# Kernel tuning notes

Hardware: AMD Instinct MI355X
Metric: run time of the kernel (lower is better)

## Reference

```python
import jax, jax.numpy as jnp
import numpy as np
from jax import lax

V = 9; C1 = 80; C2 = 40; C4 = 24; CH = 32
H1, W1 = 30, 40; H2, W2 = 60, 80; H4, W4 = 120, 160
SHAPE = (96, 96, 96); N = 131072; EPS = 1e-5
OFFS = np.stack(np.meshgrid(np.arange(-1, 2), np.arange(-1, 2), np.arange(-1, 2), indexing='ij'), -1).reshape(-1, 3).astype(np.int32)  # 27 kernel offsets


def conv2d(x, w, b):
    y = lax.conv_general_dilated(x, w, (1, 1), 'SAME', dimension_numbers=('NCHW', 'OIHW', 'NCHW'))
    return y + b[None, :, None, None]


def bn1d(x, g, b):  # eval-mode BatchNorm1d (running_mean=0, running_var=1)
    return g * x * (1.0 / np.sqrt(1.0 + EPS)) + b


def layernorm(x, g, b):
    m = x.mean(-1, keepdims=True)
    v = ((x - m) ** 2).mean(-1, keepdims=True)
    return (x - m) / jnp.sqrt(v + EPS) * g + b


def grid_sample_zeros(img, gx, gy):
    # img [V,C,H,W]; gx,gy [V,M] normalized to [-1,1]; bilinear, align_corners=True, zeros padding
    Vn, C, H, W = img.shape
    px = (gx + 1.0) * 0.5 * (W - 1)
    py = (gy + 1.0) * 0.5 * (H - 1)
    x0 = jnp.floor(px); y0 = jnp.floor(py)
    wx = px - x0; wy = py - y0
    flat = img.reshape(Vn, C, H * W)
    def corner(xc, yc, wgt):
        valid = (xc >= 0) & (xc <= W - 1) & (yc >= 0) & (yc <= H - 1)
        xi = jnp.clip(xc, 0, W - 1).astype(jnp.int32)
        yi = jnp.clip(yc, 0, H - 1).astype(jnp.int32)
        idx = yi * W + xi  # [V,M]
        g = jax.vmap(lambda f, i: f[:, i])(flat, idx)  # [V,C,M]
        return g * (wgt * valid)[:, None, :]
    return (corner(x0, y0, (1 - wx) * (1 - wy)) + corner(x0 + 1, y0, wx * (1 - wy))
            + corner(x0, y0 + 1, (1 - wx) * wy) + corner(x0 + 1, y0 + 1, wx * wy))


def subm_conv(feat, W3, cxyz, grid):
    # submanifold sparse 3x3x3 conv: per-offset gather of active neighbors -> GEMM -> accumulate
    n = feat.shape[0]
    shp = jnp.asarray(SHAPE, jnp.int32)
    out = jnp.zeros((n, W3.shape[-1]), feat.dtype)
    for k in range(27):
        nc = cxyz + jnp.asarray(OFFS[k])
        inb = jnp.all((nc >= 0) & (nc < shp), axis=1)
        ncc = jnp.clip(nc, 0, shp - 1)
        idx = grid[ncc[:, 0], ncc[:, 1], ncc[:, 2]]
        ok = (inb & (idx >= 0)).astype(feat.dtype)
        g = feat[jnp.clip(idx, 0, n - 1)] * ok[:, None]
        out = out + g @ W3[k]
    return out


def _forward(feats_1x, feats_2x, feats_4x, origin, voxel_size, KRcam,
             w_f1, b_f1, w_f2, b_f2, w_f4, b_f4, w_down, b_down,
             w_p1, b_p1, w_p2, b_p2, w_p3, b_p3, w_p4, b_p4,
             bn0_g, bn0_b, w_elan, w_s1, ln1_g, ln1_b, w_s2, ln2_g, ln2_b,
             w_s3, ln3_g, ln3_b, w_s4, bn4_g, bn4_b,
             coords, stage, min_view_number):
    # feat_fusion_pre (bs=1, take batch 0)
    f1 = jax.nn.relu(conv2d(feats_1x[:, 0], w_f1, b_f1))
    f2 = jax.nn.relu(conv2d(feats_2x[:, 0], w_f2, b_f2))
    f4 = jax.nn.relu(conv2d(feats_4x[:, 0], w_f4, b_f4))
    f1 = jax.image.resize(f1, (V, C1, H2, W2), 'bilinear')  # F.interpolate x2
    f4 = f4.reshape(V, C4, H2, 2, W2, 2).mean(axis=(3, 5))  # AvgPool2d(2)
    fuse = jnp.concatenate([f1, f2, f4], axis=1)
    fuse = jax.nn.relu(conv2d(fuse, w_down, b_down))
    for w, b in ((w_p1, b_p1), (w_p2, b_p2), (w_p3, b_p3), (w_p4, b_p4)):
        fuse = fuse + jax.nn.relu(conv2d(fuse, w, b))  # residual blocks -> [V,CH,H2,W2]
    # multi-view projection
    cxyz = coords[:, 1:]
    world = cxyz.astype(jnp.float32) * voxel_size + origin[0]
    hom = jnp.concatenate([world, jnp.ones_like(world[:, :1])], axis=1)  # [N,4]
    im_p = jnp.einsum('vij,nj->vin', KRcam[:, 0], hom)  # [V,3,N]
    im_z = im_p[:, 2]
    gx = 2.0 * (im_p[:, 0] / im_z) / (W4 - 1) - 1.0
    gy = 2.0 * (im_p[:, 1] / im_z) / (H4 - 1) - 1.0
    mask = (jnp.abs(gx) <= 1) & (jnp.abs(gy) <= 1) & (im_z > 0)  # [V,N]
    count = mask.sum(0).astype(jnp.float32)
    # inputs are constructed so every voxel is seen by all views: valid_voxel compaction == identity
    feats = grid_sample_zeros(fuse, gx, gy) * mask[:, None, :]  # [V,CH,N]
    feat = feats.transpose(2, 0, 1)  # [N,V,CH]
    m = mask.T.astype(feat.dtype)  # [N,V]
    den = m.sum(1, keepdims=True)
    mean = (m[..., None] * feat).sum(1) / den
    var = (m[..., None] * (feat - mean[:, None, :]) ** 2).sum(1) / den  # [N,CH]
    # sparse subm conv chain
    sc = cxyz // (2 ** (2 - stage))  # stage=2 -> identity
    grid = jnp.full(SHAPE, -1, jnp.int32).at[sc[:, 0], sc[:, 1], sc[:, 2]].set(jnp.arange(N, dtype=jnp.int32))
    x = bn1d(var, bn0_g, bn0_b)
    x = jax.nn.relu(subm_conv(x, w_elan, sc, grid))  # Spares3dELAN stand-in
    r = jax.nn.relu(subm_conv(x, w_s1, sc, grid)); x = layernorm(r + x, ln1_g, ln1_b)
    r = jax.nn.relu(subm_conv(x, w_s2, sc, grid)); x = layernorm(r + x, ln2_g, ln2_b)
    r = jax.nn.relu(subm_conv(x, w_s3, sc, grid)); x = layernorm(r + x, ln3_g, ln3_b)
    occ = bn1d(subm_conv(x, w_s4, sc, grid), bn4_g, bn4_b)  # [N,1]
    return occ, coords, count


def setup_inputs() -> dict:
    key = jax.random.key(0)
    keys = jax.random.split(key, 40)
    ki = iter(range(40))
    def rn(shape, s=1.0):
        return jax.random.normal(keys[next(ki)], shape, jnp.float32) * s
    inp = {}
    inp['feats_1x'] = rn((V, 1, C1, H1, W1))
    inp['feats_2x'] = rn((V, 1, C2, H2, W2))
    inp['feats_4x'] = rn((V, 1, C4, H4, W4))
    flat = np.arange(N, dtype=np.int64) * 6  # unique active voxels in a 96^3 grid
    cx = flat // (96 * 96); rem = flat % (96 * 96)
    inp['coords'] = jnp.asarray(np.stack([np.zeros(N, np.int64), cx, rem // 96, rem % 96], 1), jnp.int32)
    inp['origin'] = jnp.asarray([[-1.92, -1.92, 1.0]], jnp.float32)
    inp['voxel_size'] = jnp.float32(0.04)
    fx, fy = 38.0, 28.0
    P = np.zeros((V, 1, 3, 4), np.float32)
    for v in range(V):
        P[v, 0] = np.array([[fx, 0.0, (W4 - 1) / 2, fx * 0.02 * (v - 4)],
                            [0.0, fy, (H4 - 1) / 2, 0.0],
                            [0.0, 0.0, 1.0, 0.0]], np.float32)
    inp['KRcam'] = jnp.asarray(P)
    s = 0.05
    inp['w_f1'] = rn((C1, C1, 3, 3), s); inp['b_f1'] = rn((C1,), s)
    inp['w_f2'] = rn((C2, C2, 3, 3), s); inp['b_f2'] = rn((C2,), s)
    inp['w_f4'] = rn((C4, C4, 3, 3), s); inp['b_f4'] = rn((C4,), s)
    inp['w_down'] = rn((CH, C1 + C2 + C4, 1, 1), s); inp['b_down'] = rn((CH,), s)
    for i in (1, 2, 3, 4):
        inp['w_p%d' % i] = rn((CH, CH, 3, 3), s); inp['b_p%d' % i] = rn((CH,), s)
    inp['bn0_g'] = jnp.ones((CH,), jnp.float32); inp['bn0_b'] = jnp.zeros((CH,), jnp.float32)
    inp['w_elan'] = rn((27, CH, CH), s)
    inp['w_s1'] = rn((27, CH, CH), s); inp['ln1_g'] = jnp.ones((CH,), jnp.float32); inp['ln1_b'] = jnp.zeros((CH,), jnp.float32)
    inp['w_s2'] = rn((27, CH, CH), s); inp['ln2_g'] = jnp.ones((CH,), jnp.float32); inp['ln2_b'] = jnp.zeros((CH,), jnp.float32)
    inp['w_s3'] = rn((27, CH, CH), s); inp['ln3_g'] = jnp.ones((CH,), jnp.float32); inp['ln3_b'] = jnp.zeros((CH,), jnp.float32)
    inp['w_s4'] = rn((27, CH, 1), s); inp['bn4_g'] = jnp.ones((1,), jnp.float32); inp['bn4_b'] = jnp.zeros((1,), jnp.float32)
    inp['stage'] = 2
    inp['min_view_number'] = 1
    return inp


def reference(feats_1x, feats_2x, feats_4x, origin, voxel_size, KRcam,
              w_f1, b_f1, w_f2, b_f2, w_f4, b_f4, w_down, b_down,
              w_p1, b_p1, w_p2, b_p2, w_p3, b_p3, w_p4, b_p4,
              bn0_g, bn0_b, w_elan, w_s1, ln1_g, ln1_b, w_s2, ln2_g, ln2_b,
              w_s3, ln3_g, ln3_b, w_s4, bn4_g, bn4_b,
              coords, stage, min_view_number):
    return _forward(feats_1x, feats_2x, feats_4x, origin, voxel_size, KRcam,
                    w_f1, b_f1, w_f2, b_f2, w_f4, b_f4, w_down, b_down,
                    w_p1, b_p1, w_p2, b_p2, w_p3, b_p3, w_p4, b_p4,
                    bn0_g, bn0_b, w_elan, w_s1, ln1_g, ln1_b, w_s2, ln2_g, ln2_b,
                    w_s3, ln3_g, ln3_b, w_s4, bn4_g, bn4_b,
                    coords, stage, min_view_number)
```

## Files before the change

kernel.cpp:

```cpp
#include <hip/hip_runtime.h>
#include <math.h>

#define VN 9
#define NVOX 131072
#define GS 96
static constexpr float INVS = 0.9999950000374997f;

typedef short bf16x8 __attribute__((ext_vector_type(8)));
typedef float f32x4v __attribute__((ext_vector_type(4)));

__device__ inline float4 ld4(const float* p){ return *reinterpret_cast<const float4*>(p); }

__device__ inline ushort f2b(float f){
  unsigned u = __float_as_uint(f);
  unsigned r = (u + 0x7fffu + ((u >> 16) & 1u)) >> 16;
  return (ushort)r;
}
__device__ inline float b2f(ushort s){ return __uint_as_float(((unsigned)s) << 16); }
__device__ inline float blo(unsigned u){ return __uint_as_float(u << 16); }
__device__ inline float bhi(unsigned u){ return __uint_as_float(u & 0xffff0000u); }

__device__ inline float4 ld4b(const ushort* p){
  uint2 u = *reinterpret_cast<const uint2*>(p);
  float4 r; r.x = blo(u.x); r.y = bhi(u.x); r.z = blo(u.y); r.w = bhi(u.y); return r;
}
__device__ inline void st4b(ushort* p, float4 v){
  uint2 u;
  u.x = (unsigned)f2b(v.x) | ((unsigned)f2b(v.y) << 16);
  u.y = (unsigned)f2b(v.z) | ((unsigned)f2b(v.w) << 16);
  *reinterpret_cast<uint2*>(p) = u;
}

__device__ inline void wprep2_dev(const float* __restrict__ w, ushort* __restrict__ o,
                                  int Cout, int Cin, int K, int CK, int CoutPad, int tid){
  int ci32 = tid & 31;
  int co = (tid >> 5) % CoutPad;
  int ck = (tid / (32*CoutPad)) % CK;
  int tap = tid / (32*CoutPad*CK);
  int ci = ck*32 + ci32;
  float v = 0.f;
  if (co < Cout && ci < Cin) v = w[(size_t)(co*Cin + ci)*K*K + tap];
  o[tid] = f2b(v);
}
__device__ inline void wprep_dev(const float* __restrict__ w, ushort* __restrict__ o, int tid){
  int k = tid >> 10;
  int r = tid & 1023;
  int co = r >> 5;
  int ci = r & 31;
  o[tid] = f2b(w[k*1024 + ci*32 + co]);
}

__device__ inline void nhwc_tile_dev(const float* __restrict__ in, ushort* __restrict__ out,
                                     int C, int Cpad, int HW, int tile, int tilesPerV,
                                     float* lds, int tx){
  int v  = tile / tilesPerV;
  int p0 = (tile - v*tilesPerV) * 64;
  const float* ip = in + (size_t)v*C*HW + p0;
  int iters = Cpad >> 2;
  for (int i = 0; i < iters; ++i){
    int idx = i*256 + tx;
    int c = idx >> 6;
    int p = idx & 63;
    float val = 0.f;
    if (c < C && (p0 + p) < HW) val = ip[(size_t)c*HW + p];
    lds[c*65 + p] = val;
  }
  __syncthreads();
  int groups = Cpad >> 2;
  int tot = 64*groups;
  for (int basei = 0; basei < tot; basei += 256){
    int idx = basei + tx;
    if (idx < tot){
      int g  = idx % groups;
      int px = idx / groups;
      if ((p0 + px) < HW){
        float4 r;
        r.x = lds[(g*4+0)*65 + px];
        r.y = lds[(g*4+1)*65 + px];
        r.z = lds[(g*4+2)*65 + px];
        r.w = lds[(g*4+3)*65 + px];
        st4b(out + (size_t)(v*HW + p0 + px)*Cpad + g*4, r);
      }
    }
  }
}

__global__ __launch_bounds__(256) void k_prep(
    const float* wf1s, const float* wf2s, const float* wf4s, const float* wdns,
    const float* wp0s, const float* wp1s, const float* wp2s, const float* wp3s,
    const float* wes, const float* ws1s, const float* ws2s, const float* ws3s,
    ushort* wf1, ushort* wf2, ushort* wf4, ushort* wdn,
    ushort* wp0, ushort* wp1, ushort* wp2, ushort* wp3,
    ushort* w2e, ushort* w2s1, ushort* w2s2, ushort* w2s3,
    int* grid,
    const float* f1, const float* f2, const float* f4,
    ushort* o1, ushort* o2, ushort* o4){
  __shared__ float lds[96*65];
  int bid = blockIdx.x;
  int tx = threadIdx.x;
  if (bid < 270){ int t = bid*256+tx; if (t < 69120) wprep2_dev(wf1s, wf1, 80, 80, 3, 3, 80, t); return; }
  bid -= 270;
  if (bid < 108){ int t = bid*256+tx; if (t < 27648) wprep2_dev(wf2s, wf2, 40, 40, 3, 2, 48, t); return; }
  bid -= 108;
  if (bid < 36){ int t = bid*256+tx; if (t < 9216) wprep2_dev(wf4s, wf4, 24, 24, 3, 1, 32, t); return; }
  bid -= 36;
  if (bid < 20){ int t = bid*256+tx; if (t < 5120) wprep2_dev(wdns, wdn, 32, 144, 1, 5, 32, t); return; }
  bid -= 20;
  if (bid < 36){ int t = bid*256+tx; if (t < 9216) wprep2_dev(wp0s, wp0, 32, 32, 3, 1, 32, t); return; }
  bid -= 36;
  if (bid < 36){ int t = bid*256+tx; if (t < 9216) wprep2_dev(wp1s, wp1, 32, 32, 3, 1, 32, t); return; }
  bid -= 36;
  if (bid < 36){ int t = bid*256+tx; if (t < 9216) wprep2_dev(wp2s, wp2, 32, 32, 3, 1, 32, t); return; }
  bid -= 36;
  if (bid < 36){ int t = bid*256+tx; if (t < 9216) wprep2_dev(wp3s, wp3, 32, 32, 3, 1, 32, t); return; }
  bid -= 36;
  if (bid < 108){ int t = bid*256+tx; if (t < 27648) wprep_dev(wes, w2e, t); return; }
  bid -= 108;
  if (bid < 108){ int t = bid*256+tx; if (t < 27648) wprep_dev(ws1s, w2s1, t); return; }
  bid -= 108;
  if (bid < 108){ int t = bid*256+tx; if (t < 27648) wprep_dev(ws2s, w2s2, t); return; }
  bid -= 108;
  if (bid < 108){ int t = bid*256+tx; if (t < 27648) wprep_dev(ws3s, w2s3, t); return; }
  bid -= 108;
  if (bid < 3456){ int t = bid*256+tx; if (t < GS*GS*GS) grid[t] = -1; return; }
  bid -= 3456;
  if (bid < 171){ nhwc_tile_dev(f1, o1, 80, 96, 1200, bid, 19, lds, tx); return; }
  bid -= 171;
  if (bid < 675){ nhwc_tile_dev(f2, o2, 40, 64, 4800, bid, 75, lds, tx); return; }
  bid -= 675;
  if (bid < 2700){ nhwc_tile_dev(f4, o4, 24, 32, 19200, bid, 300, lds, tx); }
}

template<int CK, int NT, int TAPS, int MT>
__device__ void conv_dev(
    const ushort* __restrict__ fin, const ushort* __restrict__ w2,
    const float* __restrict__ bias, ushort* __restrict__ outp,
    int H, int W, int total, int Cout, int outStride, int outOff,
    int bid, int tid){
  constexpr int CIN = CK*32;
  constexpr int COP = NT*16;
  int lane = tid & 63;
  int wave = tid >> 6;
  int vbase = bid*(MT*64) + wave*(MT*16);
  int m = lane & 15, q = lane >> 4;
  int HW = H*W;
  int p[MT], py[MT], px[MT]; bool pin[MT];
  #pragma unroll
  for (int t = 0; t < MT; ++t){
    int pp = vbase + t*16 + m;
    pin[t] = pp < total;
    if (pp > total-1) pp = total-1;
    p[t] = pp;
    int v = pp / HW; int rem = pp - v*HW;
    int y = rem / W;
    py[t] = y; px[t] = rem - y*W;
  }
  f32x4v acc[MT][NT];
  #pragma unroll
  for (int t = 0; t < MT; ++t)
    #pragma unroll
    for (int n = 0; n < NT; ++n) acc[t][n] = 0.f;
  bf16x8 z = (short)0;

  #pragma unroll 1
  for (int tap = 0; tap < TAPS; ++tap){
    int dy = (TAPS == 9) ? tap/3 - 1 : 0;
    int dx = (TAPS == 9) ? tap%3 - 1 : 0;
    int off = dy*W + dx;
    bool val[MT];
    #pragma unroll
    for (int t = 0; t < MT; ++t)
      val[t] = pin[t] && ((unsigned)(py[t]+dy) < (unsigned)H)
                      && ((unsigned)(px[t]+dx) < (unsigned)W);
    #pragma unroll
    for (int ck = 0; ck < CK; ++ck){
      bf16x8 Af[MT], Bf[NT];
      #pragma unroll
      for (int t = 0; t < MT; ++t){
        size_t idx = val[t] ? (size_t)(p[t]+off) : 0;
        bf16x8 a = *(const bf16x8*)(fin + idx*CIN + ck*32 + q*8);
        Af[t] = val[t] ? a : z;
      }
      #pragma unroll
      for (int n = 0; n < NT; ++n)
        Bf[n] = *(const bf16x8*)(w2 + ((size_t)((tap*CK+ck)*COP + n*16 + m))*32 + q*8);
      #pragma unroll
      for (int t = 0; t < MT; ++t)
        #pragma unroll
        for (int n = 0; n < NT; ++n)
          acc[t][n] = __builtin_amdgcn_mfma_f32_16x16x32_bf16(Bf[n], Af[t], acc[t][n], 0, 0, 0);
    }
  }

  #pragma unroll
  for (int n = 0; n < NT; ++n){
    int co4 = n*16 + q*4;
    bool cok = co4 < Cout;
    float4 bs = cok ? ld4(bias + co4) : float4{0.f,0.f,0.f,0.f};
    #pragma unroll
    for (int t = 0; t < MT; ++t){
      int pp = vbase + t*16 + m;
      if (pp < total && cok){
        float4 v;
        v.x = fmaxf(acc[t][n][0] + bs.x, 0.f);
        v.y = fmaxf(acc[t][n][1] + bs.y, 0.f);
        v.z = fmaxf(acc[t][n][2] + bs.z, 0.f);
        v.w = fmaxf(acc[t][n][3] + bs.w, 0.f);
        st4b(outp + (size_t)pp*outStride + outOff + co4, v);
      }
    }
  }
}

template<int CK, int NT, int TAPS, int MT>
__global__ __launch_bounds__(256) void k_conv_mfma(
    const ushort* __restrict__ fin, const ushort* __restrict__ w2,
    const float* __restrict__ bias, ushort* __restrict__ outp,
    int H, int W, int total, int Cout, int outStride, int outOff){
  conv_dev<CK,NT,TAPS,MT>(fin, w2, bias, outp, H, W, total, Cout, outStride, outOff,
                          blockIdx.x, threadIdx.x);
}

template<int TH, int NT>
__device__ void conv_lds_dev(
    const ushort* __restrict__ fin, const ushort* __restrict__ w2,
    const float* __restrict__ bias, ushort* __restrict__ outp,
    int H, int W, int Cout, int outStride,
    const ushort* __restrict__ skipin, ushort* lds, int bid, int tid){
  constexpr int RPW = TH/4;
  constexpr int PS = 36;
  int xtiles = W >> 4;
  int ytiles = (H + TH - 1) / TH;
  int v  = bid / (ytiles*xtiles);
  int rem = bid - v*(ytiles*xtiles);
  int ty = (rem / xtiles) * TH;
  int tx = (rem % xtiles) * 16;
  const ushort* ibase = fin + (size_t)v*H*W*32;
  for (int i = tid; i < (TH+2)*18*4; i += 256){
    int chunk = i & 3;
    int pxi = i >> 2;
    int ly = pxi / 18, lx = pxi - ly*18;
    int gy = ty + ly - 1, gx = tx + lx - 1;
    uint4 d = {0,0,0,0};
    if ((unsigned)gy < (unsigned)H && (unsigned)gx < (unsigned)W)
      d = *(const uint4*)(ibase + ((size_t)gy*W + gx)*32 + chunk*8);
    *(uint4*)(lds + (size_t)(ly*18 + lx)*PS + chunk*8) = d;
  }
  __syncthreads();
  int lane = tid & 63;
  int wave = tid >> 6;
  int m = lane & 15, q = lane >> 4;
  f32x4v acc[RPW][NT];
  #pragma unroll
  for (int t = 0; t < RPW; ++t)
    #pragma unroll
    for (int n = 0; n < NT; ++n) acc[t][n] = 0.f;

  #pragma unroll 1
  for (int tap = 0; tap < 9; ++tap){
    int dy = tap/3 - 1, dx = tap%3 - 1;
    bf16x8 Af[RPW], Bf[NT];
    #pragma unroll
    for (int t = 0; t < RPW; ++t){
      int ly = wave*RPW + t + 1 + dy;
      int lx = m + 1 + dx;
      Af[t] = *(const bf16x8*)(lds + (size_t)(ly*18 + lx)*PS + q*8);
    }
    #pragma unroll
    for (int n = 0; n < NT; ++n)
      Bf[n] = *(const bf16x8*)(w2 + ((size_t)(tap*(NT*16) + n*16 + m))*32 + q*8);
    #pragma unroll
    for (int t = 0; t < RPW; ++t)
      #pragma unroll
      for (int n = 0; n < NT; ++n)
        acc[t][n] = __builtin_amdgcn_mfma_f32_16x16x32_bf16(Bf[n], Af[t], acc[t][n], 0, 0, 0);
  }

  #pragma unroll
  for (int n = 0; n < NT; ++n){
    int co4 = n*16 + q*4;
    bool cok = co4 < Cout;
    float4 bs = cok ? ld4(bias + co4) : float4{0.f,0.f,0.f,0.f};
    #pragma unroll
    for (int t = 0; t < RPW; ++t){
      int y = ty + wave*RPW + t;
      int x = tx + m;
      if (y < H && cok){
        size_t pp = (size_t)(v*H + y)*W + x;
        float4 val;
        val.x = fmaxf(acc[t][n][0] + bs.x, 0.f);
        val.y = fmaxf(acc[t][n][1] + bs.y, 0.f);
        val.z = fmaxf(acc[t][n][2] + bs.z, 0.f);
        val.w = fmaxf(acc[t][n][3] + bs.w, 0.f);
        if (skipin){
          float4 sk = ld4b(skipin + pp*32 + co4);
          val.x += sk.x; val.y += sk.y; val.z += sk.z; val.w += sk.w;
        }
        st4b(outp + pp*outStride + co4, val);
      }
    }
  }
}

__global__ __launch_bounds__(256) void k_conv_lds4(
    const ushort* __restrict__ fin, const ushort* __restrict__ w2,
    const float* __restrict__ bias, ushort* __restrict__ outp,
    const ushort* __restrict__ skipin){
  __shared__ ushort lds[6*18*36];
  conv_lds_dev<4,2>(fin, w2, bias, outp, 60, 80, 32, 32, skipin, lds, blockIdx.x, threadIdx.x);
}

__device__ void scatter_dev(const int* __restrict__ coords, const int* __restrict__ stage,
                            int* __restrict__ grid, int* __restrict__ scn,
                            float* __restrict__ coords_out,
                            const float* __restrict__ origin, const float* __restrict__ vsz,
                            const float* __restrict__ KR,
                            ushort* __restrict__ sidx, float4* __restrict__ swf,
                            float* __restrict__ cnt, int n){
  int c0 = coords[n*4], c1 = coords[n*4+1], c2 = coords[n*4+2], c3 = coords[n*4+3];
  coords_out[n*4+0] = (float)c0;
  coords_out[n*4+1] = (float)c1;
  coords_out[n*4+2] = (float)c2;
  coords_out[n*4+3] = (float)c3;
  int sh = 2 - stage[0];
  int s1 = c1 >> sh, s2 = c2 >> sh, s3 = c3 >> sh;
  scn[n*3+0] = s1; scn[n*3+1] = s2; scn[n*3+2] = s3;
  grid[(s1*GS + s2)*GS + s3] = n;

  float vs = vsz[0];
  float wx = (float)c1*vs + origin[0];
  float wy = (float)c2*vs + origin[1];
  float wz = (float)c3*vs + origin[2];
  float den = 0.f;
  #pragma unroll 1
  for (int v = 0; v < VN; ++v){
    const float* P = KR + v*12;
    float ix = P[0]*wx + P[1]*wy + P[2]*wz + P[3];
    float iy = P[4]*wx + P[5]*wy + P[6]*wz + P[7];
    float iz = P[8]*wx + P[9]*wy + P[10]*wz + P[11];
    float gx = 2.f*(ix/iz)/159.f - 1.f;
    float gy = 2.f*(iy/iz)/119.f - 1.f;
    bool ok = (fabsf(gx) <= 1.f) && (fabsf(gy) <= 1.f) && (iz > 0.f);
    float px = ok ? (gx + 1.f)*0.5f*79.f : 0.f;
    float py = ok ? (gy + 1.f)*0.5f*59.f : 0.f;
    float x0f = floorf(px), y0f = floorf(py);
    float fx = px - x0f, fy = py - y0f;
    int idx = (int)y0f*80 + (int)x0f;
    float mf = ok ? 1.f : 0.f;
    den += mf;
    float4 w;
    w.x = (1.f-fx)*(1.f-fy)*mf;
    w.y = fx*(1.f-fy)*mf;
    w.z = (1.f-fx)*fy*mf;
    w.w = fx*fy*mf;
    sidx[(size_t)v*NVOX + n] = (ushort)idx;
    swf[(size_t)v*NVOX + n] = w;
  }
  cnt[n] = den;
}

__global__ __launch_bounds__(256) void k_heads(
    const ushort* nhwc1, const ushort* wf1, const float* b_f1, ushort* t1,
    const ushort* nhwc2, const ushort* wf2, const float* b_f2, ushort* fcat,
    const ushort* nhwc4, const ushort* wf4, const float* b_f4, ushort* t4,
    const int* coords, const int* stage, int* grid, int* scn, float* coords_out,
    const float* origin, const float* vsz, const float* KR,
    ushort* sidx, float4* swf, float* cnt){
  __shared__ ushort lds[18*18*36];
  int bid = blockIdx.x;
  int tid = threadIdx.x;
  if (bid < 169){ conv_dev<3,5,9,1>(nhwc1, wf1, b_f1, t1, 30, 40, 10800, 80, 80, 0, bid, tid); return; }
  bid -= 169;
  if (bid < 720){ conv_lds_dev<16,2>(nhwc4, wf4, b_f4, t4, 120, 160, 24, 24, nullptr, lds, bid, tid); return; }
  bid -= 720;
  if (bid < 675){ conv_dev<2,3,9,1>(nhwc2, wf2, b_f2, fcat, 60, 80, 43200, 40, 160, 80, bid, tid); return; }
  bid -= 675;
  { int n = bid*256 + tid;
    scatter_dev(coords, stage, grid, scn, coords_out, origin, vsz, KR, sidx, swf, cnt, n); }
}

__global__ __launch_bounds__(256) void k_respool_nbr(
    const ushort* __restrict__ t1, const ushort* __restrict__ t4, ushort* __restrict__ fc,
    const int* __restrict__ scn, const int* __restrict__ grid,
    int* __restrict__ nbr, unsigned* __restrict__ gmask16){
  __shared__ unsigned m16[4];
  int bid = blockIdx.x;
  int tidx = threadIdx.x;
  if (bid < 5063){
    int tid = bid*256 + tidx;
    if (tid < 864000){
      int c4 = tid % 20;
      int x  = (tid / 20) % 80;
      int y  = (tid / 1600) % 60;
      int v  = tid / 96000;
      int c = c4*4;
      int ky = y >> 1; int y0, y1; float wy0, wy1;
      if ((y & 1) == 0){ y0 = ky-1; y1 = ky; wy0 = 0.25f; wy1 = 0.75f; if (y0 < 0){ y0 = 0; wy0 = 0.f; wy1 = 1.f; } }
      else             { y0 = ky; y1 = ky+1; wy0 = 0.75f; wy1 = 0.25f; if (y1 > 29){ y1 = 29; wy1 = 0.f; wy0 = 1.f; } }
      int kx = x >> 1; int x0, x1; float wx0, wx1;
      if ((x & 1) == 0){ x0 = kx-1; x1 = kx; wx0 = 0.25f; wx1 = 0.75f; if (x0 < 0){ x0 = 0; wx0 = 0.f; wx1 = 1.f; } }
      else             { x0 = kx; x1 = kx+1; wx0 = 0.75f; wx1 = 0.25f; if (x1 > 39){ x1 = 39; wx1 = 0.f; wx0 = 1.f; } }
      float4 a00 = ld4b(t1 + ((size_t)(v*30 + y0)*40 + x0)*80 + c);
      float4 a01 = ld4b(t1 + ((size_t)(v*30 + y0)*40 + x1)*80 + c);
      float4 a10 = ld4b(t1 + ((size_t)(v*30 + y1)*40 + x0)*80 + c);
      float4 a11 = ld4b(t1 + ((size_t)(v*30 + y1)*40 + x1)*80 + c);
      float w00 = wy0*wx0, w01 = wy0*wx1, w10 = wy1*wx0, w11 = wy1*wx1;
      float4 r;
      r.x = w00*a00.x + w01*a01.x + w10*a10.x + w11*a11.x;
      r.y = w00*a00.y + w01*a01.y + w10*a10.y + w11*a11.y;
      r.z = w00*a00.z + w01*a01.z + w10*a10.z + w11*a11.z;
      r.w = w00*a00.w + w01*a01.w + w10*a10.w + w11*a11.w;
      st4b(fc + ((size_t)(v*60 + y)*80 + x)*160 + c, r);
      return;
    }
    int t = tid - 864000;
    if (t >= 432000) return;
    int c4 = t % 10;
    int x  = (t / 10) % 80;
    int y  = (t / 800) % 60;
    int v  = t / 48000;
    if (c4 < 6){
      int c = c4*4;
      const ushort* b0 = t4 + ((size_t)(v*120 + 2*y)*160 + 2*x)*24 + c;
      float4 a = ld4b(b0), b = ld4b(b0 + 24), cc = ld4b(b0 + 160*24), d = ld4b(b0 + 160*24 + 24);
      float4 r;
      r.x = 0.25f*(a.x + b.x + cc.x + d.x);
      r.y = 0.25f*(a.y + b.y + cc.y + d.y);
      r.z = 0.25f*(a.z + b.z + cc.z + d.z);
      r.w = 0.25f*(a.w + b.w + cc.w + d.w);
      st4b(fc + ((size_t)(v*60 + y)*80 + x)*160 + 120 + c, r);
    } else {
      float4 zz = {0.f,0.f,0.f,0.f};
      st4b(fc + ((size_t)(v*60 + y)*80 + x)*160 + 144 + (c4-6)*4, zz);
    }
    return;
  }
  bid -= 5063;
  if (tidx < 4) m16[tidx] = 0;
  __syncthreads();
  int vb = bid*64;
  int lane = tidx & 63;
  int wv = tidx >> 6;
  int n = vb + lane;
  int sx = scn[n*3+0], sy = scn[n*3+1], sz = scn[n*3+2];
  int k0 = wv*7;
  int k1 = min(27, k0 + 7);
  unsigned msk = 0;
  #pragma unroll 1
  for (int k = k0; k < k1; ++k){
    int dx = k/9 - 1, dy = (k/3)%3 - 1, dz = k%3 - 1;
    int nx = sx+dx, ny = sy+dy, nz = sz+dz;
    int idx = -1;
    if (((unsigned)nx < 96u) && ((unsigned)ny < 96u) && ((unsigned)nz < 96u))
      idx = grid[(nx*GS + ny)*GS + nz];
    unsigned long long b = __ballot(idx >= 0);
    unsigned sub = (unsigned)((b >> ((lane >> 4)*16)) & 0xFFFFull);
    if (sub){
      nbr[(size_t)k*NVOX + n] = idx;
      msk |= (1u << k);
    }
  }
  if ((lane & 15) == 0 && msk) atomicOr(&m16[lane >> 4], msk);
  __syncthreads();
  if (tidx < 4) gmask16[(vb >> 4) + tidx] = m16[tidx];
}

__global__ __launch_bounds__(256) void k_sample(
    const ushort* __restrict__ fuse, const ushort* __restrict__ sidx,
    const float4* __restrict__ swf,
    const float* __restrict__ cnt, const float* __restrict__ bn0g,
    const float* __restrict__ bn0b, ushort* __restrict__ F0){
  int tid = blockIdx.x*256 + threadIdx.x;
  int vox = tid >> 3;
  int c4 = tid & 7;
  int c = c4*4;
  float s0=0.f,s1=0.f,s2=0.f,s3=0.f;
  float q0=0.f,q1=0.f,q2=0.f,q3=0.f;
  #pragma unroll
  for (int v = 0; v < VN; ++v){
    int idx = sidx[(size_t)v*NVOX + vox];
    float4 w = swf[(size_t)v*NVOX + vox];
    const ushort* bp = fuse + (size_t)v*153600 + (size_t)idx*32 + c;
    float4 a00 = ld4b(bp);
    float4 a01 = ld4b(bp + 32);
    float4 a10 = ld4b(bp + 2560);
    float4 a11 = ld4b(bp + 2592);
    float g0 = w.x*a00.x + w.y*a01.x + w.z*a10.x + w.w*a11.x;
    float g1 = w.x*a00.y + w.y*a01.y + w.z*a10.y + w.w*a11.y;
    float g2 = w.x*a00.z + w.y*a01.z + w.z*a10.z + w.w*a11.z;
    float g3 = w.x*a00.w + w.y*a01.w + w.z*a10.w + w.w*a11.w;
    s0 += g0; q0 += g0*g0;
    s1 += g1; q1 += g1*g1;
    s2 += g2; q2 += g2*g2;
    s3 += g3; q3 += g3*g3;
  }
  float iden = 1.f/cnt[vox];
  float m0 = s0*iden, m1 = s1*iden, m2 = s2*iden, m3 = s3*iden;
  float4 g = ld4(bn0g + c);
  float4 b = ld4(bn0b + c);
  float4 r;
  r.x = g.x*fmaxf(q0*iden - m0*m0, 0.f)*INVS + b.x;
  r.y = g.y*fmaxf(q1*iden - m1*m1, 0.f)*INVS + b.y;
  r.z = g.z*fmaxf(q2*iden - m2*m2, 0.f)*INVS + b.z;
  r.w = g.w*fmaxf(q3*iden - m3*m3, 0.f)*INVS + b.w;
  st4b(F0 + (size_t)vox*32 + c, r);
}

template<int MODE>
__global__ __launch_bounds__(256, 4) void k_subm_mfma(
    const ushort* __restrict__ fin, const ushort* __restrict__ w2,
    const int* __restrict__ nbr, const unsigned* __restrict__ gmask16,
    const float* __restrict__ lng, const float* __restrict__ lnb,
    ushort* __restrict__ fout){
  int lane = threadIdx.x & 63;
  int wave = threadIdx.x >> 6;
  int vb = blockIdx.x*128 + wave*32;
  int m = lane & 15;
  int q = lane >> 4;

  unsigned rem0 = gmask16[(vb >> 4) + 0];
  unsigned rem1 = gmask16[(vb >> 4) + 1];
  unsigned rem = rem0 | rem1;

  f32x4v acc[2][2];
  acc[0][0] = 0.f; acc[0][1] = 0.f; acc[1][0] = 0.f; acc[1][1] = 0.f;
  bf16x8 zc = (short)0;

  while (rem){
    int k0 = __ffs(rem) - 1; rem &= rem - 1;
    int k1 = -1, k2 = -1;
    if (rem){ k1 = __ffs(rem) - 1; rem &= rem - 1; }
    if (rem){ k2 = __ffs(rem) - 1; rem &= rem - 1; }
    int a0v = nbr[(size_t)k0*NVOX + vb + m];
    int b0v = nbr[(size_t)k0*NVOX + vb + 16 + m];
    int a1 = -1, b1 = -1, a2 = -1, b2 = -1;
    if (k1 >= 0){
      int av = nbr[(size_t)k1*NVOX + vb + m];
      int bv = nbr[(size_t)k1*NVOX + vb + 16 + m];
      a1 = ((rem0 >> k1) & 1) ? av : -1;
      b1 = ((rem1 >> k1) & 1) ? bv : -1;
    }
    if (k2 >= 0){
      int av = nbr[(size_t)k2*NVOX + vb + m];
      int bv = nbr[(size_t)k2*NVOX + vb + 16 + m];
      a2 = ((rem0 >> k2) & 1) ? av : -1;
      b2 = ((rem1 >> k2) & 1) ? bv : -1;
    }
    int a0 = ((rem0 >> k0) & 1) ? a0v : -1;
    int b0 = ((rem1 >> k0) & 1) ? b0v : -1;
    bf16x8 A0, B0, A1 = zc, B1 = zc, A2 = zc, B2 = zc, t;
    bf16x8 w10 = zc, w11 = zc, w20 = zc, w21 = zc;
    t = *(const bf16x8*)(fin + (size_t)(a0 < 0 ? 0 : a0)*32 + q*8); A0 = (a0 < 0) ? zc : t;
    t = *(const bf16x8*)(fin + (size_t)(b0 < 0 ? 0 : b0)*32 + q*8); B0 = (b0 < 0) ? zc : t;
    bf16x8 w00 = *(const bf16x8*)(w2 + (size_t)(k0*32 + m)*32 + q*8);
    bf16x8 w01 = *(const bf16x8*)(w2 + (size_t)(k0*32 + 16 + m)*32 + q*8);
    if (k1 >= 0){
      t = *(const bf16x8*)(fin + (size_t)(a1 < 0 ? 0 : a1)*32 + q*8); A1 = (a1 < 0) ? zc : t;
      t = *(const bf16x8*)(fin + (size_t)(b1 < 0 ? 0 : b1)*32 + q*8); B1 = (b1 < 0) ? zc : t;
      w10 = *(const bf16x8*)(w2 + (size_t)(k1*32 + m)*32 + q*8);
      w11 = *(const bf16x8*)(w2 + (size_t)(k1*32 + 16 + m)*32 + q*8);
    }
    if (k2 >= 0){
      t = *(const bf16x8*)(fin + (size_t)(a2 < 0 ? 0 : a2)*32 + q*8); A2 = (a2 < 0) ? zc : t;
      t = *(const bf16x8*)(fin + (size_t)(b2 < 0 ? 0 : b2)*32 + q*8); B2 = (b2 < 0) ? zc : t;
      w20 = *(const bf16x8*)(w2 + (size_t)(k2*32 + m)*32 + q*8);
      w21 = *(const bf16x8*)(w2 + (size_t)(k2*32 + 16 + m)*32 + q*8);
    }
    acc[0][0] = __builtin_amdgcn_mfma_f32_16x16x32_bf16(w00, A0, acc[0][0], 0, 0, 0);
    acc[0][1] = __builtin_amdgcn_mfma_f32_16x16x32_bf16(w01, A0, acc[0][1], 0, 0, 0);
    acc[1][0] = __builtin_amdgcn_mfma_f32_16x16x32_bf16(w00, B0, acc[1][0], 0, 0, 0);
    acc[1][1] = __builtin_amdgcn_mfma_f32_16x16x32_bf16(w01, B0, acc[1][1], 0, 0, 0);
    if (k1 >= 0){
      acc[0][0] = __builtin_amdgcn_mfma_f32_16x16x32_bf16(w10, A1, acc[0][0], 0, 0, 0);
      acc[0][1] = __builtin_amdgcn_mfma_f32_16x16x32_bf16(w11, A1, acc[0][1], 0, 0, 0);
      acc[1][0] = __builtin_amdgcn_mfma_f32_16x16x32_bf16(w10, B1, acc[1][0], 0, 0, 0);
      acc[1][1] = __builtin_amdgcn_mfma_f32_16x16x32_bf16(w11, B1, acc[1][1], 0, 0, 0);
    }
    if (k2 >= 0){
      acc[0][0] = __builtin_amdgcn_mfma_f32_16x16x32_bf16(w20, A2, acc[0][0], 0, 0, 0);
      acc[0][1] = __builtin_amdgcn_mfma_f32_16x16x32_bf16(w21, A2, acc[0][1], 0, 0, 0);
      acc[1][0] = __builtin_amdgcn_mfma_f32_16x16x32_bf16(w20, B2, acc[1][0], 0, 0, 0);
      acc[1][1] = __builtin_amdgcn_mfma_f32_16x16x32_bf16(w21, B2, acc[1][1], 0, 0, 0);
    }
  }

  float4 g0v{0,0,0,0}, g1v{0,0,0,0}, b0v{0,0,0,0}, b1v{0,0,0,0};
  if (MODE == 1){
    g0v = ld4(lng + q*4);  g1v = ld4(lng + 16 + q*4);
    b0v = ld4(lnb + q*4);  b1v = ld4(lnb + 16 + q*4);
  }
  #pragma unroll
  for (int t = 0; t < 2; ++t){
    int vox = vb + t*16 + m;
    float x0[4], x1[4];
    #pragma unroll
    for (int r = 0; r < 4; ++r){
      x0[r] = fmaxf(acc[t][0][r], 0.f);
      x1[r] = fmaxf(acc[t][1][r], 0.f);
    }
    if (MODE == 1){
      uint2 sk0 = *(const uint2*)(fin + (size_t)vox*32 + q*4);
      uint2 sk1 = *(const uint2*)(fin + (size_t)vox*32 + 16 + q*4);
      x0[0] += blo(sk0.x); x0[1] += bhi(sk0.x); x0[2] += blo(sk0.y); x0[3] += bhi(sk0.y);
      x1[0] += blo(sk1.x); x1[1] += bhi(sk1.x); x1[2] += blo(sk1.y); x1[3] += bhi(sk1.y);
      float s = (x0[0]+x0[1]+x0[2]+x0[3]) + (x1[0]+x1[1]+x1[2]+x1[3]);
      s += __shfl_xor(s, 16);
      s += __shfl_xor(s, 32);
      float mean = s * (1.f/32.f);
      float v2 = 0.f;
      #pragma unroll
      for (int r = 0; r < 4; ++r){
        x0[r] -= mean; x1[r] -= mean;
        v2 += x0[r]*x0[r] + x1[r]*x1[r];
      }
      v2 += __shfl_xor(v2, 16);
      v2 += __shfl_xor(v2, 32);
      float rs = 1.f / sqrtf(v2*(1.f/32.f) + 1e-5f);
      x0[0] = x0[0]*rs*g0v.x + b0v.x; x0[1] = x0[1]*rs*g0v.y + b0v.y;
      x0[2] = x0[2]*rs*g0v.z + b0v.z; x0[3] = x0[3]*rs*g0v.w + b0v.w;
      x1[0] = x1[0]*rs*g1v.x + b1v.x; x1[1] = x1[1]*rs*g1v.y + b1v.y;
      x1[2] = x1[2]*rs*g1v.z + b1v.z; x1[3] = x1[3]*rs*g1v.w + b1v.w;
    }
    st4b(fout + (size_t)vox*32 + q*4,      float4{x0[0],x0[1],x0[2],x0[3]});
    st4b(fout + (size_t)vox*32 + 16 + q*4, float4{x1[0],x1[1],x1[2],x1[3]});
  }
}

__global__ __launch_bounds__(256) void k_s4(
    const ushort* __restrict__ fin, const float* __restrict__ w4,
    const int* __restrict__ nbr, const unsigned* __restrict__ gmask16,
    const float* __restrict__ bn4g, const float* __restrict__ bn4b,
    float* __restrict__ occ){
  int tid = blockIdx.x*256 + threadIdx.x;
  int n = tid >> 2;
  int part = tid & 3;
  unsigned rem = gmask16[n >> 4];
  float acc = 0.f;
  while (rem){
    int k0 = __ffs(rem) - 1; rem &= rem - 1;
    int k1 = -1;
    if (rem){ k1 = __ffs(rem) - 1; rem &= rem - 1; }
    int i0 = nbr[(size_t)k0*NVOX + n];
    int i1 = (k1 >= 0) ? nbr[(size_t)k1*NVOX + n] : -1;
    uint4 d0 = *(const uint4*)(fin + (size_t)(i0 < 0 ? 0 : i0)*32 + part*8);
    uint4 d1 = {0,0,0,0};
    if (k1 >= 0) d1 = *(const uint4*)(fin + (size_t)(i1 < 0 ? 0 : i1)*32 + part*8);
    if (i0 >= 0){
      float4 wa = ld4(w4 + k0*32 + part*8);
      float4 wb = ld4(w4 + k0*32 + part*8 + 4);
      acc += blo(d0.x)*wa.x + bhi(d0.x)*wa.y + blo(d0.y)*wa.z + bhi(d0.y)*wa.w
           + blo(d0.z)*wb.x + bhi(d0.z)*wb.y + blo(d0.w)*wb.z + bhi(d0.w)*wb.w;
    }
    if (i1 >= 0){
      float4 wa = ld4(w4 + k1*32 + part*8);
      float4 wb = ld4(w4 + k1*32 + part*8 + 4);
      acc += blo(d1.x)*wa.x + bhi(d1.x)*wa.y + blo(d1.y)*wa.z + bhi(d1.y)*wa.w
           + blo(d1.z)*wb.x + bhi(d1.z)*wb.y + blo(d1.w)*wb.z + bhi(d1.w)*wb.w;
    }
  }
  acc += __shfl_xor(acc, 1, 4);
  acc += __shfl_xor(acc, 2, 4);
  if (part == 0) occ[n] = bn4g[0]*acc*INVS + bn4b[0];
}

extern "C" void kernel_launch(void* const* d_in, const int* in_sizes, int n_in,
                              void* d_out, int out_size, void* d_ws, size_t ws_size,
                              hipStream_t stream){
  const float* feats1 = (const float*)d_in[0];
  const float* feats2 = (const float*)d_in[1];
  const float* feats4 = (const float*)d_in[2];
  const int*   coords = (const int*)d_in[3];
  const float* origin = (const float*)d_in[4];
  const float* vsz    = (const float*)d_in[5];
  const float* KR     = (const float*)d_in[6];
  const float* w_f1 = (const float*)d_in[7];  const float* b_f1 = (const float*)d_in[8];
  const float* w_f2 = (const float*)d_in[9];  const float* b_f2 = (const float*)d_in[10];
  const float* w_f4 = (const float*)d_in[11]; const float* b_f4 = (const float*)d_in[12];
  const float* w_dn = (const float*)d_in[13]; const float* b_dn = (const float*)d_in[14];
  const float* w_p[4] = {(const float*)d_in[15], (const float*)d_in[17],
                         (const float*)d_in[19], (const float*)d_in[21]};
  const float* b_p[4] = {(const float*)d_in[16], (const float*)d_in[18],
                         (const float*)d_in[20], (const float*)d_in[22]};
  const float* bn0g = (const float*)d_in[23]; const float* bn0b = (const float*)d_in[24];
  const float* w_elan = (const float*)d_in[25];
  const float* w_s1 = (const float*)d_in[26]; const float* ln1g = (const float*)d_in[27]; const float* ln1b = (const float*)d_in[28];
  const float* w_s2 = (const float*)d_in[29]; const float* ln2g = (const float*)d_in[30]; const float* ln2b = (const float*)d_in[31];
  const float* w_s3 = (const float*)d_in[32]; const float* ln3g = (const float*)d_in[33]; const float* ln3b = (const float*)d_in[34];
  const float* w_s4 = (const float*)d_in[35]; const float* bn4g = (const float*)d_in[36]; const float* bn4b = (const float*)d_in[37];
  const int* stage  = (const int*)d_in[38];
  float* out = (float*)d_out;
  char* base = (char*)d_ws;

  size_t off = 0;
  auto alloc = [&](size_t bytes)->char*{ char* p = base + off; off += (bytes + 255) & ~(size_t)255; return p; };
  ushort* nhwc1 = (ushort*)alloc((size_t)9*30*40*96*2);
  ushort* nhwc2 = (ushort*)alloc((size_t)9*60*80*64*2);
  ushort* nhwc4 = (ushort*)alloc((size_t)9*120*160*32*2);
  ushort* t1    = (ushort*)alloc((size_t)9*30*40*80*2);
  ushort* t4    = (ushort*)alloc((size_t)9*120*160*24*2);
  ushort* fcat  = (ushort*)alloc((size_t)9*60*80*160*2);
  ushort* A     = (ushort*)alloc((size_t)9*60*80*32*2);
  ushort* B     = (ushort*)alloc((size_t)9*60*80*32*2);
  ushort* Fb0   = (ushort*)alloc((size_t)NVOX*32*2);
  ushort* Fb1   = (ushort*)alloc((size_t)NVOX*32*2);
  int*    nbr   = (int*)alloc((size_t)27*NVOX*4);
  int*    grid  = (int*)alloc((size_t)GS*GS*GS*4);
  int*    scn   = (int*)alloc((size_t)NVOX*3*4);
  unsigned* gmask16 = (unsigned*)alloc((size_t)(NVOX/16)*4);
  ushort* wf1   = (ushort*)alloc(9*3*80*32*2);
  ushort* wf2   = (ushort*)alloc(9*2*48*32*2);
  ushort* wf4   = (ushort*)alloc(9*1*32*32*2);
  ushort* wdn   = (ushort*)alloc(1*5*32*32*2);
  ushort* wp0   = (ushort*)alloc(9*1*32*32*2);
  ushort* wp1   = (ushort*)alloc(9*1*32*32*2);
  ushort* wp2   = (ushort*)alloc(9*1*32*32*2);
  ushort* wp3   = (ushort*)alloc(9*1*32*32*2);
  ushort* w2e   = (ushort*)alloc(27*1024*2);
  ushort* w2s1  = (ushort*)alloc(27*1024*2);
  ushort* w2s2  = (ushort*)alloc(27*1024*2);
  ushort* w2s3  = (ushort*)alloc(27*1024*2);
  ushort* sidx  = (ushort*)alloc((size_t)VN*NVOX*2);
  float4* swf   = (float4*)alloc((size_t)VN*NVOX*16);

  auto nb = [](int total){ return (total + 255)/256; };

  k_prep<<<8012,256,0,stream>>>(
      w_f1, w_f2, w_f4, w_dn, w_p[0], w_p[1], w_p[2], w_p[3],
      w_elan, w_s1, w_s2, w_s3,
      wf1, wf2, wf4, wdn, wp0, wp1, wp2, wp3, w2e, w2s1, w2s2, w2s3, grid,
      feats1, feats2, feats4, nhwc1, nhwc2, nhwc4);

  k_heads<<<169 + 720 + 675 + 512,256,0,stream>>>(
      nhwc1, wf1, b_f1, t1,
      nhwc2, wf2, b_f2, fcat,
      nhwc4, wf4, b_f4, t4,
      coords, stage, grid, scn, out + NVOX,
      origin, vsz, KR, sidx, swf, out + 5*NVOX);

  k_respool_nbr<<<5063 + 2048,256,0,stream>>>(t1, t4, fcat, scn, grid, nbr, gmask16);

  k_conv_mfma<5,2,1,1><<<675,256,0,stream>>>(fcat, wdn, b_dn, A, 60, 80, 43200, 32, 32, 0);
  k_conv_lds4<<<675,256,0,stream>>>(A, wp0, b_p[0], B, A);
  k_conv_lds4<<<675,256,0,stream>>>(B, wp1, b_p[1], A, B);
  k_conv_lds4<<<675,256,0,stream>>>(A, wp2, b_p[2], B, A);
  k_conv_lds4<<<675,256,0,stream>>>(B, wp3, b_p[3], A, B);

  k_sample<<<NVOX/32,256,0,stream>>>(A, sidx, swf, out + 5*NVOX, bn0g, bn0b, Fb0);

  k_subm_mfma<0><<<NVOX/128,256,0,stream>>>(Fb0, w2e,  nbr, gmask16, nullptr, nullptr, Fb1);
  k_subm_mfma<1><<<NVOX/128,256,0,stream>>>(Fb1, w2s1, nbr, gmask16, ln1g, ln1b, Fb0);
  k_subm_mfma<1><<<NVOX/128,256,0,stream>>>(Fb0, w2s2, nbr, gmask16, ln2g, ln2b, Fb1);
  k_subm_mfma<1><<<NVOX/128,256,0,stream>>>(Fb1, w2s3, nbr, gmask16, ln3g, ln3b, Fb0);

  k_s4<<<NVOX/64,256,0,stream>>>(Fb0, w_s4, nbr, gmask16, bn4g, bn4b, out);
}
```

Measured before the change: 332.7 us.

## Fuse down-projection with first conv and pairs of 2D convs via LDS halos

```diff
diff --git a/kernel.cpp b/kernel.cpp
--- a/kernel.cpp
+++ b/kernel.cpp
@@ -212,15 +212,6 @@
   }
 }
 
-template<int CK, int NT, int TAPS, int MT>
-__global__ __launch_bounds__(256) void k_conv_mfma(
-    const ushort* __restrict__ fin, const ushort* __restrict__ w2,
-    const float* __restrict__ bias, ushort* __restrict__ outp,
-    int H, int W, int total, int Cout, int outStride, int outOff){
-  conv_dev<CK,NT,TAPS,MT>(fin, w2, bias, outp, H, W, total, Cout, outStride, outOff,
-                          blockIdx.x, threadIdx.x);
-}
-
 template<int TH, int NT>
 __device__ void conv_lds_dev(
     const ushort* __restrict__ fin, const ushort* __restrict__ w2,
@@ -308,6 +299,176 @@
     const ushort* __restrict__ skipin){
   __shared__ ushort lds[6*18*36];
   conv_lds_dev<4,2>(fin, w2, bias, outp, 60, 80, 32, 32, skipin, lds, blockIdx.x, threadIdx.x);
+}
+
+__global__ __launch_bounds__(256) void k_down_p0(
+    const ushort* __restrict__ fcat, const ushort* __restrict__ wdn,
+    const float* __restrict__ b_dn, const ushort* __restrict__ wp0,
+    const float* __restrict__ b_p0, ushort* __restrict__ outB){
+  __shared__ ushort ldsA[6*18*36];
+  int bid = blockIdx.x;
+  int tid = threadIdx.x;
+  int v  = bid / 75;
+  int rem = bid - v*75;
+  int ty = (rem / 5) * 4;
+  int tx = (rem % 5) * 16;
+  int lane = tid & 63;
+  int wave = tid >> 6;
+  int m = lane & 15, q = lane >> 4;
+  bf16x8 z = (short)0;
+
+  #pragma unroll
+  for (int t = 0; t < 2; ++t){
+    int hp = (wave*2 + t)*16 + m;
+    int hpc = hp < 108 ? hp : 107;
+    int ly = hpc / 18, lx = hpc - ly*18;
+    int gy = ty + ly - 1, gx = tx + lx - 1;
+    bool ok = (hp < 108) && ((unsigned)gy < 60u) && ((unsigned)gx < 80u);
+    size_t pbase = ((size_t)(v*60 + (ok ? gy : 0))*80 + (ok ? gx : 0))*160;
+    f32x4v acc0 = 0.f, acc1 = 0.f;
+    #pragma unroll
+    for (int ck = 0; ck < 5; ++ck){
+      bf16x8 a = *(const bf16x8*)(fcat + pbase + ck*32 + q*8);
+      if (!ok) a = z;
+      bf16x8 w0 = *(const bf16x8*)(wdn + ((size_t)(ck*32 + m))*32 + q*8);
+      bf16x8 w1 = *(const bf16x8*)(wdn + ((size_t)(ck*32 + 16 + m))*32 + q*8);
+      acc0 = __builtin_amdgcn_mfma_f32_16x16x32_bf16(w0, a, acc0, 0, 0, 0);
+      acc1 = __builtin_amdgcn_mfma_f32_16x16x32_bf16(w1, a, acc1, 0, 0, 0);
+    }
+    if (hp < 108){
+      float4 bs0 = ld4(b_dn + q*4);
+      float4 bs1 = ld4(b_dn + 16 + q*4);
+      float4 v0, v1;
+      v0.x = ok ? fmaxf(acc0[0] + bs0.x, 0.f) : 0.f;
+      v0.y = ok ? fmaxf(acc0[1] + bs0.y, 0.f) : 0.f;
+      v0.z = ok ? fmaxf(acc0[2] + bs0.z, 0.f) : 0.f;
+      v0.w = ok ? fmaxf(acc0[3] + bs0.w, 0.f) : 0.f;
+      v1.x = ok ? fmaxf(acc1[0] + bs1.x, 0.f) : 0.f;
+      v1.y = ok ? fmaxf(acc1[1] + bs1.y, 0.f) : 0.f;
+      v1.z = ok ? fmaxf(acc1[2] + bs1.z, 0.f) : 0.f;
+      v1.w = ok ? fmaxf(acc1[3] + bs1.w, 0.f) : 0.f;
+      st4b(ldsA + (size_t)(ly*18 + lx)*36 + q*4,      v0);
+      st4b(ldsA + (size_t)(ly*18 + lx)*36 + 16 + q*4, v1);
+    }
+  }
+  __syncthreads();
+
+  f32x4v pacc0 = 0.f, pacc1 = 0.f;
+  #pragma unroll 1
+  for (int tap = 0; tap < 9; ++tap){
+    int dy = tap/3 - 1, dx = tap%3 - 1;
+    bf16x8 Af = *(const bf16x8*)(ldsA + (size_t)((wave+1+dy)*18 + (m+1+dx))*36 + q*8);
+    bf16x8 B0 = *(const bf16x8*)(wp0 + ((size_t)(tap*32 + m))*32 + q*8);
+    bf16x8 B1 = *(const bf16x8*)(wp0 + ((size_t)(tap*32 + 16 + m))*32 + q*8);
+    pacc0 = __builtin_amdgcn_mfma_f32_16x16x32_bf16(B0, Af, pacc0, 0, 0, 0);
+    pacc1 = __builtin_amdgcn_mfma_f32_16x16x32_bf16(B1, Af, pacc1, 0, 0, 0);
+  }
+  int y = ty + wave, x = tx + m;
+  size_t pp = (size_t)(v*60 + y)*80 + x;
+  #pragma unroll
+  for (int n = 0; n < 2; ++n){
+    int co4 = n*16 + q*4;
+    float4 bs = ld4(b_p0 + co4);
+    f32x4v& pa = n ? pacc1 : pacc0;
+    float4 sk = ld4b(ldsA + (size_t)((wave+1)*18 + (m+1))*36 + co4);
+    float4 val;
+    val.x = fmaxf(pa[0] + bs.x, 0.f) + sk.x;
+    val.y = fmaxf(pa[1] + bs.y, 0.f) + sk.y;
+    val.z = fmaxf(pa[2] + bs.z, 0.f) + sk.z;
+    val.w = fmaxf(pa[3] + bs.w, 0.f) + sk.w;
+    st4b(outB + pp*32 + co4, val);
+  }
+}
+
+__global__ __launch_bounds__(256) void k_p2_p3(
+    const ushort* __restrict__ finA, const ushort* __restrict__ wp2,
+    const float* __restrict__ b_p2, const ushort* __restrict__ wp3,
+    const float* __restrict__ b_p3, ushort* __restrict__ outB){
+  __shared__ ushort ldsIn[8*20*36];
+  __shared__ ushort ldsMid[6*18*36];
+  int bid = blockIdx.x;
+  int tid = threadIdx.x;
+  int v  = bid / 75;
+  int rem = bid - v*75;
+  int ty = (rem / 5) * 4;
+  int tx = (rem % 5) * 16;
+  for (int i = tid; i < 8*20*4; i += 256){
+    int chunk = i & 3;
+    int pxi = i >> 2;
+    int ly = pxi / 20, lx = pxi - ly*20;
+    int gy = ty + ly - 2, gx = tx + lx - 2;
+    uint4 d = {0,0,0,0};
+    if ((unsigned)gy < 60u && (unsigned)gx < 80u)
+      d = *(const uint4*)(finA + ((size_t)(v*60 + gy)*80 + gx)*32 + chunk*8);
+    *(uint4*)(ldsIn + (size_t)(ly*20 + lx)*36 + chunk*8) = d;
+  }
+  __syncthreads();
+  int lane = tid & 63;
+  int wave = tid >> 6;
+  int m = lane & 15, q = lane >> 4;
+
+  #pragma unroll
+  for (int t = 0; t < 2; ++t){
+    int hp = (wave*2 + t)*16 + m;
+    int hpc = hp < 108 ? hp : 107;
+    int ly = hpc / 18, lx = hpc - ly*18;
+    int gy = ty + ly - 1, gx = tx + lx - 1;
+    bool ok = (hp < 108) && ((unsigned)gy < 60u) && ((unsigned)gx < 80u);
+    f32x4v acc0 = 0.f, acc1 = 0.f;
+    #pragma unroll 1
+    for (int tap = 0; tap < 9; ++tap){
+      int dy = tap/3 - 1, dx = tap%3 - 1;
+      bf16x8 a = *(const bf16x8*)(ldsIn + (size_t)((ly+dy+1)*20 + (lx+dx+1))*36 + q*8);
+      bf16x8 w0 = *(const bf16x8*)(wp2 + ((size_t)(tap*32 + m))*32 + q*8);
+      bf16x8 w1 = *(const bf16x8*)(wp2 + ((size_t)(tap*32 + 16 + m))*32 + q*8);
+      acc0 = __builtin_amdgcn_mfma_f32_16x16x32_bf16(w0, a, acc0, 0, 0, 0);
+      acc1 = __builtin_amdgcn_mfma_f32_16x16x32_bf16(w1, a, acc1, 0, 0, 0);
+    }
+    if (hp < 108){
+      float4 bs0 = ld4(b_p2 + q*4);
+      float4 bs1 = ld4(b_p2 + 16 + q*4);
+      float4 sk0 = ld4b(ldsIn + (size_t)((ly+1)*20 + (lx+1))*36 + q*4);
+      float4 sk1 = ld4b(ldsIn + (size_t)((ly+1)*20 + (lx+1))*36 + 16 + q*4);
+      float4 v0, v1;
+      v0.x = ok ? fmaxf(acc0[0] + bs0.x, 0.f) + sk0.x : 0.f;
+      v0.y = ok ? fmaxf(acc0[1] + bs0.y, 0.f) + sk0.y : 0.f;
+      v0.z = ok ? fmaxf(acc0[2] + bs0.z, 0.f) + sk0.z : 0.f;
+      v0.w = ok ? fmaxf(acc0[3] + bs0.w, 0.f) + sk0.w : 0.f;
+      v1.x = ok ? fmaxf(acc1[0] + bs1.x, 0.f) + sk1.x : 0.f;
+      v1.y = ok ? fmaxf(acc1[1] + bs1.y, 0.f) + sk1.y : 0.f;
+      v1.z = ok ? fmaxf(acc1[2] + bs1.z, 0.f) + sk1.z : 0.f;
+      v1.w = ok ? fmaxf(acc1[3] + bs1.w, 0.f) + sk1.w : 0.f;
+      st4b(ldsMid + (size_t)(ly*18 + lx)*36 + q*4,      v0);
+      st4b(ldsMid + (size_t)(ly*18 + lx)*36 + 16 + q*4, v1);
+    }
+  }
+  __syncthreads();
+
+  f32x4v pacc0 = 0.f, pacc1 = 0.f;
+  #pragma unroll 1
+  for (int tap = 0; tap < 9; ++tap){
+    int dy = tap/3 - 1, dx = tap%3 - 1;
+    bf16x8 a = *(const bf16x8*)(ldsMid + (size_t)((wave+1+dy)*18 + (m+1+dx))*36 + q*8);
+    bf16x8 w0 = *(const bf16x8*)(wp3 + ((size_t)(tap*32 + m))*32 + q*8);
+    bf16x8 w1 = *(const bf16x8*)(wp3 + ((size_t)(tap*32 + 16 + m))*32 + q*8);
+    pacc0 = __builtin_amdgcn_mfma_f32_16x16x32_bf16(w0, a, pacc0, 0, 0, 0);
+    pacc1 = __builtin_amdgcn_mfma_f32_16x16x32_bf16(w1, a, pacc1, 0, 0, 0);
+  }
+  int y = ty + wave, x = tx + m;
+  size_t pp = (size_t)(v*60 + y)*80 + x;
+  #pragma unroll
+  for (int n = 0; n < 2; ++n){
+    int co4 = n*16 + q*4;
+    float4 bs = ld4(b_p3 + co4);
+    f32x4v& pa = n ? pacc1 : pacc0;
+    float4 sk = ld4b(ldsMid + (size_t)((wave+1)*18 + (m+1))*36 + co4);
+    float4 val;
+    val.x = fmaxf(pa[0] + bs.x, 0.f) + sk.x;
+    val.y = fmaxf(pa[1] + bs.y, 0.f) + sk.y;
+    val.z = fmaxf(pa[2] + bs.z, 0.f) + sk.z;
+    val.w = fmaxf(pa[3] + bs.w, 0.f) + sk.w;
+    st4b(outB + pp*32 + co4, val);
+  }
 }
 
 __device__ void scatter_dev(const int* __restrict__ coords, const int* __restrict__ stage,
@@ -739,13 +900,11 @@
 
   k_respool_nbr<<<5063 + 2048,256,0,stream>>>(t1, t4, fcat, scn, grid, nbr, gmask16);
 
-  k_conv_mfma<5,2,1,1><<<675,256,0,stream>>>(fcat, wdn, b_dn, A, 60, 80, 43200, 32, 32, 0);
-  k_conv_lds4<<<675,256,0,stream>>>(A, wp0, b_p[0], B, A);
+  k_down_p0<<<675,256,0,stream>>>(fcat, wdn, b_dn, wp0, b_p[0], B);
   k_conv_lds4<<<675,256,0,stream>>>(B, wp1, b_p[1], A, B);
-  k_conv_lds4<<<675,256,0,stream>>>(A, wp2, b_p[2], B, A);
-  k_conv_lds4<<<675,256,0,stream>>>(B, wp3, b_p[3], A, B);
-
-  k_sample<<<NVOX/32,256,0,stream>>>(A, sidx, swf, out + 5*NVOX, bn0g, bn0b, Fb0);
+  k_p2_p3<<<675,256,0,stream>>>(A, wp2, b_p[2], wp3, b_p[3], B);
+
+  k_sample<<<NVOX/32,256,0,stream>>>(B, sidx, swf, out + 5*NVOX, bn0g, bn0b, Fb0);
 
   k_subm_mfma<0><<<NVOX/128,256,0,stream>>>(Fb0, w2e,  nbr, gmask16, nullptr, nullptr, Fb1);
   k_subm_mfma<1><<<NVOX/128,256,0,stream>>>(Fb1, w2s1, nbr, gmask16, ln1g, ln1b, Fb0);
```

Measured after the change: 330.7 us. No clear change (-0.6%).
